# Performance work log

Hardware: AMD Instinct MI355X
Metric: run time of the kernel (lower is better)

Reference implementation:

```python
import jax, jax.numpy as jnp
import numpy as np

B, S, D = 2, 2048, 1024
H = 16
HD = D // H  # 64


def setup_inputs() -> dict:
    key = jax.random.key(0)
    ks = jax.random.split(key, 6)
    x = jax.random.normal(ks[0], (B, S, D), dtype=jnp.float32)
    sc = 1.0 / np.sqrt(D)
    Wq = jax.random.normal(ks[1], (D, D), dtype=jnp.float32) * sc
    Wk = jax.random.normal(ks[2], (D, D), dtype=jnp.float32) * sc
    Wv = jax.random.normal(ks[3], (D, D), dtype=jnp.float32) * sc
    Wo = jax.random.normal(ks[4], (D, D), dtype=jnp.float32) * sc
    bo = jax.random.normal(ks[5], (D,), dtype=jnp.float32) * 0.01
    return {"x": x, "Wq": Wq, "Wk": Wk, "Wv": Wv, "Wo": Wo, "bo": bo}


def reference(x, Wq, Wk, Wv, Wo, bo):
    b, s, d = x.shape
    # projections (torch Linear: y = x @ W.T; weights here stored as [d_in, d_out])
    Q = (x @ Wq).reshape(b, s, H, HD).transpose(0, 2, 1, 3)  # [b,h,s,hd]
    K = (x @ Wk).reshape(b, s, H, HD).transpose(0, 2, 1, 3)
    V = (x @ Wv).reshape(b, s, H, HD).transpose(0, 2, 1, 3)
    scores = jnp.einsum("bhqd,bhkd->bhqk", Q, K) / np.sqrt(HD)
    causal = jnp.triu(jnp.ones((s, s), dtype=bool), k=1)  # True above diagonal
    scores = jnp.where(causal[None, None], -jnp.inf, scores)
    attn = jax.nn.softmax(scores, axis=-1)
    # dropout_rate = 0.0 -> identity (eval-mode reference)
    ctx = jnp.einsum("bhqk,bhkd->bhqd", attn, V)
    ctx = ctx.transpose(0, 2, 1, 3).reshape(b, s, d)
    return ctx @ Wo + bo
```

## Files before the change

### kernel.cpp

```cpp
#include <hip/hip_runtime.h>
#include <hip/hip_bf16.h>

#define B_  2
#define S_  2048
#define D_  1024
#define H_  16
#define HD_ 64
#define M_  (B_*S_)

typedef __attribute__((ext_vector_type(8))) short short8;
typedef __attribute__((ext_vector_type(4))) float f32x4;

#define MFMA16(a, b, c) __builtin_amdgcn_mfma_f32_16x16x32_bf16((a), (b), (c), 0, 0, 0)

static __device__ inline short f2bf(float f) {
    union { float f; unsigned u; } v; v.f = f;
    unsigned r = v.u + 0x7FFFu + ((v.u >> 16) & 1u);
    return (short)(r >> 16);
}

static __device__ __forceinline__ float fexp2(float x) {
    float r;
    asm volatile("v_exp_f32 %0, %1\n\ts_nop 1" : "=v"(r) : "v"(x));
    return r;
}

static __device__ __forceinline__ unsigned cvt_pk_bf16(float lo, float hi) {
    unsigned r;
    asm volatile("v_cvt_pk_bf16_f32 %0, %1, %2" : "=v"(r) : "v"(lo), "v"(hi));
    return r;
}

static __device__ __forceinline__ void gl_lds16(const short* g, short* l) {
    __builtin_amdgcn_global_load_lds(
        (const __attribute__((address_space(1))) void*)g,
        (__attribute__((address_space(3))) void*)l, 16, 0, 0);
}

__global__ void cvt_x_kernel(const float* __restrict__ x, short* __restrict__ xb, int n4) {
    int i = blockIdx.x * blockDim.x + threadIdx.x;
    int stride = gridDim.x * blockDim.x;
    for (; i < n4; i += stride) {
        float4 v = ((const float4*)x)[i];
        short4 o;
        o.x = f2bf(v.x); o.y = f2bf(v.y); o.z = f2bf(v.z); o.w = f2bf(v.w);
        ((short4*)xb)[i] = o;
    }
}

__global__ void transpose_w4_kernel(const float* __restrict__ Wq, const float* __restrict__ Wk,
                                    const float* __restrict__ Wv, const float* __restrict__ Wo,
                                    short* __restrict__ Wqkvt, short* __restrict__ Wot) {
    __shared__ float tile[32][33];
    int z = blockIdx.z;
    const float* W = (z == 0) ? Wq : (z == 1) ? Wk : (z == 2) ? Wv : Wo;
    short* Wt = (z == 3) ? Wot : (Wqkvt + ((size_t)z << 20));
    int tx = threadIdx.x & 31, ty = threadIdx.x >> 5;
    int n0 = blockIdx.x * 32, k0 = blockIdx.y * 32;
#pragma unroll
    for (int i = 0; i < 4; ++i)
        tile[ty + 8 * i][tx] = W[(size_t)(k0 + ty + 8 * i) * D_ + n0 + tx];
    __syncthreads();
#pragma unroll
    for (int i = 0; i < 4; ++i)
        Wt[(size_t)(n0 + ty + 8 * i) * D_ + k0 + tx] = f2bf(tile[tx][ty + 8 * i]);
}

template <int MODE>
__global__ __launch_bounds__(256, 6) void gemm64(const short* __restrict__ A,
                                                 const short* __restrict__ Bt,
                                                 const float* __restrict__ bias,
                                                 void* __restrict__ out) {
    __shared__ __align__(16) short Asm[2][64 * 32];
    __shared__ __align__(16) short Bsm[2][128 * 32];
    int x = blockIdx.x & 7, wgl = blockIdx.x >> 3;
    int bm, bn;
    if (MODE == 0) { bn = x * 3 + (wgl >> 6); bm = wgl & 63; }
    else           { bn = x;                  bm = wgl;      }
    int tid = threadIdx.x, l = tid & 63, w = tid >> 6;
    int lhi = l >> 4, llo = l & 15;

    f32x4 acc[4][2];
#pragma unroll
    for (int m = 0; m < 4; ++m)
#pragma unroll
        for (int n = 0; n < 2; ++n) acc[m][n] = (f32x4){0.f, 0.f, 0.f, 0.f};

    const short* Ag = A + (size_t)(bm * 64) * 1024;
    const short* Bg = Bt + (size_t)(bn * 128) * 1024;
    int ca = tid;
    int ra = ((ca >> 5) << 3) | (ca & 7), sa = ((ca >> 3) & 3) ^ (ra & 3);
    int cb0 = tid, cb1 = tid + 256;
    int rb0 = ((cb0 >> 5) << 3) | (cb0 & 7), sb0 = ((cb0 >> 3) & 3) ^ (rb0 & 3);
    int rb1 = ((cb1 >> 5) << 3) | (cb1 & 7), sb1 = ((cb1 >> 3) & 3) ^ (rb1 & 3);

    auto stage = [&](int buf, int k0) {
        gl_lds16(Ag + (size_t)ra * 1024 + k0 + sa * 8, &Asm[buf][ca * 8]);
        gl_lds16(Bg + (size_t)rb0 * 1024 + k0 + sb0 * 8, &Bsm[buf][cb0 * 8]);
        gl_lds16(Bg + (size_t)rb1 * 1024 + k0 + sb1 * 8, &Bsm[buf][cb1 * 8]);
    };

    int cia[4], cib[2];
#pragma unroll
    for (int m = 0; m < 4; ++m) {
        int row = m * 16 + llo;
        cia[m] = ((row >> 3) << 5) | (((lhi ^ row) & 3) << 3) | (row & 7);
    }
#pragma unroll
    for (int n = 0; n < 2; ++n) {
        int row = w * 32 + n * 16 + llo;
        cib[n] = ((row >> 3) << 5) | (((lhi ^ row) & 3) << 3) | (row & 7);
    }

    stage(0, 0);
    for (int i = 0; i < 32; ++i) {
        asm volatile("s_waitcnt vmcnt(0)" ::: "memory");
        __builtin_amdgcn_s_barrier();
        asm volatile("" ::: "memory");
        if (i + 1 < 32) stage((i + 1) & 1, (i + 1) * 32);
        int cur = i & 1;
        short8 af[4], bf[2];
#pragma unroll
        for (int m = 0; m < 4; ++m) af[m] = *(const short8*)&Asm[cur][cia[m] * 8];
#pragma unroll
        for (int n = 0; n < 2; ++n) bf[n] = *(const short8*)&Bsm[cur][cib[n] * 8];
#pragma unroll
        for (int m = 0; m < 4; ++m)
#pragma unroll
            for (int n = 0; n < 2; ++n)
                acc[m][n] = MFMA16(af[m], bf[n], acc[m][n]);
    }

    int rowb = bm * 64, colb = bn * 128 + w * 32;
#pragma unroll
    for (int m = 0; m < 4; ++m) {
#pragma unroll
        for (int n = 0; n < 2; ++n) {
            int col = colb + n * 16 + llo;
#pragma unroll
            for (int j = 0; j < 4; ++j) {
                int row = rowb + m * 16 + lhi * 4 + j;
                float v = acc[m][n][j];
                if (MODE == 2) {
                    ((float*)out)[(size_t)row * 1024 + col] = v + bias[col];
                } else {
                    int proj = col >> 10, n1 = col & 1023;
                    int h = n1 >> 6, hd = n1 & 63;
                    int b = row >> 11, s = row & 2047;
                    short* o = (short*)out;
                    size_t off;
                    if (proj == 0)
                        off = ((size_t)(b * 16 + h) * 2048 + s) * 64 + hd;
                    else if (proj == 1)
                        off = (size_t)M_ * D_ + ((size_t)(b * 16 + h) * 2048 + s) * 64 + hd;
                    else
                        off = (size_t)2 * M_ * D_ + ((size_t)(b * 16 + h) * 64 + hd) * 2048 + s;
                    o[off] = f2bf(v);
                }
            }
        }
    }
}

__global__ __launch_bounds__(512) void attn_kernel(const short* __restrict__ Q,
                                                   const short* __restrict__ Kg,
                                                   const short* __restrict__ Vt,
                                                   short* __restrict__ ctx) {
    __shared__ __align__(16) char kvbuf[2][16384];
    __shared__ __align__(16) char plds[8][2048];
    int tid = threadIdx.x, w = tid >> 6, l = tid & 63;
    int lhi = l >> 4, llo = l & 15;
    int bh = blockIdx.x & 31, qp = blockIdx.x >> 5;
    int b = bh >> 4, h = bh & 15;
    char* pb = plds[w];

    const short* Qh = Q + (size_t)bh * S_ * HD_;
    const short* Kh = Kg + (size_t)bh * S_ * HD_;
    const short* Vh = Vt + (size_t)bh * HD_ * S_;

    int qbA = qp, qbB = 15 - qp;
    int NTA = 2 * qp + 2;
    const int NT = 34;

    int srow = tid >> 3;
    int ssrc = (16 * (tid & 7)) ^ ((srow & 7) << 4);
    auto stage = [&](char* buf, int c0) {
        gl_lds16(Kh + (size_t)(c0 + srow) * HD_ + (ssrc >> 1), (short*)(buf + tid * 16));
        gl_lds16(Vh + (size_t)srow * S_ + c0 + (ssrc >> 1), (short*)(buf + 8192 + tid * 16));
    };

    f32x4 O[4];
#pragma unroll
    for (int n = 0; n < 4; ++n) O[n] = (f32x4){0.f, 0.f, 0.f, 0.f};
    float lpart[4] = {0.f, 0.f, 0.f, 0.f};

    auto writeOut = [&](int qb) {
        int qbs = qb * 128 + w * 16;
#pragma unroll
        for (int j = 0; j < 4; ++j) {
            float ls = lpart[j];
            ls += __shfl_xor(ls, 1);
            ls += __shfl_xor(ls, 2);
            ls += __shfl_xor(ls, 4);
            ls += __shfl_xor(ls, 8);
            float inv = 1.0f / ls;
            int row = qbs + lhi * 4 + j;
            size_t base = ((size_t)(b * S_ + row)) * D_ + h * HD_;
#pragma unroll
            for (int n = 0; n < 4; ++n)
                ctx[base + n * 16 + llo] = f2bf(O[n][j] * inv);
        }
    };

    const float SC = 0.18033688f;
    const float M2 = 17.312340f;

    int qbase = qbA * 128 + w * 16;
    short8 aq0 = *(const short8*)(Qh + (size_t)(qbase + llo) * HD_ + 8 * lhi);
    short8 aq1 = *(const short8*)(Qh + (size_t)(qbase + llo) * HD_ + 32 + 8 * lhi);

    stage(kvbuf[0], 0);

    for (int i = 0; i < NT; ++i) {
        asm volatile("s_waitcnt vmcnt(0)" ::: "memory");
        __builtin_amdgcn_s_barrier();
        asm volatile("" ::: "memory");
        int kt = (i < NTA) ? i : i - NTA;
        int c0 = kt * 64;
        if (i + 1 < NT) {
            int ni = i + 1;
            int nkt = (ni < NTA) ? ni : ni - NTA;
            stage(kvbuf[ni & 1], nkt * 64);
        }
        const char* kb = kvbuf[i & 1];
        const char* vb = kb + 8192;

        if (c0 <= qbase + 15) {
            f32x4 sc4[4];
#pragma unroll
            for (int cb = 0; cb < 4; ++cb) {
                int row = cb * 16 + llo;
                int sw = (row & 7) << 4;
                short8 kf0 = *(const short8*)(kb + row * 128 + ((16 * lhi) ^ sw));
                short8 kf1 = *(const short8*)(kb + row * 128 + ((64 + 16 * lhi) ^ sw));
                f32x4 z = (f32x4){0.f, 0.f, 0.f, 0.f};
                z = MFMA16(aq0, kf0, z);
                z = MFMA16(aq1, kf1, z);
                sc4[cb] = z;
            }
            bool diag = (c0 + 63 > qbase);
#pragma unroll
            for (int j = 0; j < 4; ++j) {
                int qr = qbase + lhi * 4 + j;
                float v0 = fmaf(sc4[0][j], SC, -M2);
                float v1 = fmaf(sc4[1][j], SC, -M2);
                float v2 = fmaf(sc4[2][j], SC, -M2);
                float v3 = fmaf(sc4[3][j], SC, -M2);
                if (diag) {
                    if (c0 + llo > qr)      v0 = -1e30f;
                    if (c0 + 16 + llo > qr) v1 = -1e30f;
                    if (c0 + 32 + llo > qr) v2 = -1e30f;
                    if (c0 + 48 + llo > qr) v3 = -1e30f;
                }
                float p0 = fexp2(v0), p1 = fexp2(v1);
                float p2 = fexp2(v2), p3 = fexp2(v3);
                lpart[j] += (p0 + p1) + (p2 + p3);
                unsigned pk01 = cvt_pk_bf16(p0, p1);
                unsigned pk23 = cvt_pk_bf16(p2, p3);
                int r = lhi * 4 + j;
                char* rb = pb + r * 128;
                int sw = (r & 7) << 4;
                *(short*)(rb + ((2 * llo) ^ sw))      = (short)(pk01);
                *(short*)(rb + ((2 * llo + 32) ^ sw)) = (short)(pk01 >> 16);
                *(short*)(rb + ((2 * llo + 64) ^ sw)) = (short)(pk23);
                *(short*)(rb + ((2 * llo + 96) ^ sw)) = (short)(pk23 >> 16);
            }
            int swr = (llo & 7) << 4;
            short8 pa0 = *(const short8*)(pb + llo * 128 + ((16 * lhi) ^ swr));
            short8 pa1 = *(const short8*)(pb + llo * 128 + ((64 + 16 * lhi) ^ swr));
#pragma unroll
            for (int n = 0; n < 4; ++n) {
                int row = n * 16 + llo;
                int sw = (row & 7) << 4;
                short8 vf0 = *(const short8*)(vb + row * 128 + ((16 * lhi) ^ sw));
                short8 vf1 = *(const short8*)(vb + row * 128 + ((64 + 16 * lhi) ^ sw));
                O[n] = MFMA16(pa0, vf0, O[n]);
                O[n] = MFMA16(pa1, vf1, O[n]);
            }
        }

        if (i == NTA - 1) {
            writeOut(qbA);
#pragma unroll
            for (int n = 0; n < 4; ++n) O[n] = (f32x4){0.f, 0.f, 0.f, 0.f};
            lpart[0] = lpart[1] = lpart[2] = lpart[3] = 0.f;
            qbase = qbB * 128 + w * 16;
            aq0 = *(const short8*)(Qh + (size_t)(qbase + llo) * HD_ + 8 * lhi);
            aq1 = *(const short8*)(Qh + (size_t)(qbase + llo) * HD_ + 32 + 8 * lhi);
        }
    }
    writeOut(qbB);
}

extern "C" void kernel_launch(void* const* d_in, const int* in_sizes, int n_in,
                              void* d_out, int out_size, void* d_ws, size_t ws_size,
                              hipStream_t stream) {
    const float* x  = (const float*)d_in[0];
    const float* Wq = (const float*)d_in[1];
    const float* Wk = (const float*)d_in[2];
    const float* Wv = (const float*)d_in[3];
    const float* Wo = (const float*)d_in[4];
    const float* bo = (const float*)d_in[5];
    float* out = (float*)d_out;

    char* ws = (char*)d_ws;
    short* xb    = (short*)(ws);
    short* Wqkvt = (short*)(ws + (size_t)(8 << 20));
    short* Wot   = (short*)(ws + (size_t)(14 << 20));
    short* Qb    = (short*)(ws + (size_t)(16 << 20));
    short* Kb    = Qb + (size_t)M_ * D_;
    short* Vtb   = Qb + (size_t)2 * M_ * D_;
    short* ctx   = xb;

    cvt_x_kernel<<<2048, 256, 0, stream>>>(x, xb, M_ * D_ / 4);
    transpose_w4_kernel<<<dim3(32, 32, 4), 256, 0, stream>>>(Wq, Wk, Wv, Wo, Wqkvt, Wot);

    gemm64<0><<<1536, 256, 0, stream>>>(xb, Wqkvt, nullptr, Qb);
    attn_kernel<<<256, 512, 0, stream>>>(Qb, Kb, Vtb, ctx);
    gemm64<2><<<512, 256, 0, stream>>>(ctx, Wot, bo, out);
}
```

Before: 140.2 us.

## Replace QKV projection GEMM with 256x256-tile, 8-wave kernel using K=64 stages

The fused QKV projection moves from a 64x128 tile GEMM with 1536 small blocks to a dedicated kernel with 256x256 output tiles, 512 threads (8 waves in a 2x4 grid) and K-step 64, using direct global-to-LDS loads with an XOR swizzle. Larger tiles raise arithmetic intensity and cut redundant global/L2 traffic for A and B. In exchange, only 192 blocks run (fewer than the CU count, so some CUs idle), each block needs 128KB of LDS, and register pressure is high from the 128 accumulator floats per lane. The output projection keeps the old kernel under a new non-templated name.

```diff
diff --git a/kernel.cpp b/kernel.cpp
--- a/kernel.cpp
+++ b/kernel.cpp
@@ -66,17 +66,114 @@
         Wt[(size_t)(n0 + ty + 8 * i) * D_ + k0 + tx] = f2bf(tile[tx][ty + 8 * i]);
 }
 
-template <int MODE>
-__global__ __launch_bounds__(256, 6) void gemm64(const short* __restrict__ A,
-                                                 const short* __restrict__ Bt,
-                                                 const float* __restrict__ bias,
-                                                 void* __restrict__ out) {
+__global__ __launch_bounds__(512, 2) void gemm_qkv8(const short* __restrict__ A,
+                                                    const short* __restrict__ Bt,
+                                                    short* __restrict__ out) {
+    __shared__ __align__(16) short Als[2][256 * 64];
+    __shared__ __align__(16) short Bls[2][256 * 64];
+    int x = blockIdx.x & 7, wgl = blockIdx.x >> 3;
+    int wg = x * 24 + wgl;
+    int bn = wg / 16, bm = wg % 16;
+    int tid = threadIdx.x, l = tid & 63, w = tid >> 6;
+    int lhi = l >> 4, llo = l & 15;
+    int wm = w >> 2, wn = w & 3;
+
+    f32x4 acc[8][4];
+#pragma unroll
+    for (int m = 0; m < 8; ++m)
+#pragma unroll
+        for (int n = 0; n < 4; ++n) acc[m][n] = (f32x4){0.f, 0.f, 0.f, 0.f};
+
+    const short* Ag = A + (size_t)(bm * 256) * 1024;
+    const short* Bg = Bt + (size_t)(bn * 256) * 1024;
+
+    int rowp[4], sp[4];
+#pragma unroll
+    for (int p = 0; p < 4; ++p) {
+        int c = p * 512 + tid;
+        rowp[p] = ((c >> 6) << 3) | (c & 7);
+        sp[p] = ((c >> 3) & 7) ^ (rowp[p] & 7);
+    }
+    auto cidx = [](int row, int s) {
+        return ((row >> 3) << 6) | (((s ^ row) & 7) << 3) | (row & 7);
+    };
+
+#pragma unroll
+    for (int p = 0; p < 4; ++p) {
+        gl_lds16(Ag + (size_t)rowp[p] * 1024 + sp[p] * 8, &Als[0][(p * 512 + tid) * 8]);
+        gl_lds16(Bg + (size_t)rowp[p] * 1024 + sp[p] * 8, &Bls[0][(p * 512 + tid) * 8]);
+    }
+
+    for (int t = 0; t < 16; ++t) {
+        asm volatile("s_waitcnt vmcnt(0)" ::: "memory");
+        __builtin_amdgcn_s_barrier();
+        asm volatile("" ::: "memory");
+        int cur = t & 1, nxt = cur ^ 1;
+        short8 bf[4];
+#pragma unroll
+        for (int p = 0; p < 4; ++p) {
+            if (t + 1 < 16) {
+                gl_lds16(Ag + (size_t)rowp[p] * 1024 + (t + 1) * 64 + sp[p] * 8,
+                         &Als[nxt][(p * 512 + tid) * 8]);
+                gl_lds16(Bg + (size_t)rowp[p] * 1024 + (t + 1) * 64 + sp[p] * 8,
+                         &Bls[nxt][(p * 512 + tid) * 8]);
+            }
+            int kk = p >> 1, mh = p & 1;
+            if (mh == 0) {
+#pragma unroll
+                for (int nf = 0; nf < 4; ++nf) {
+                    int row = wn * 64 + nf * 16 + llo, s = kk * 4 + lhi;
+                    bf[nf] = *(const short8*)&Bls[cur][cidx(row, s) * 8];
+                }
+            }
+            short8 af[4];
+#pragma unroll
+            for (int mf = 0; mf < 4; ++mf) {
+                int row = wm * 128 + (mh * 4 + mf) * 16 + llo, s = kk * 4 + lhi;
+                af[mf] = *(const short8*)&Als[cur][cidx(row, s) * 8];
+            }
+#pragma unroll
+            for (int mf = 0; mf < 4; ++mf)
+#pragma unroll
+                for (int nf = 0; nf < 4; ++nf)
+                    acc[mh * 4 + mf][nf] = MFMA16(af[mf], bf[nf], acc[mh * 4 + mf][nf]);
+        }
+    }
+
+    int rowb = bm * 256 + wm * 128, colb = bn * 256 + wn * 64;
+#pragma unroll
+    for (int f = 0; f < 8; ++f) {
+#pragma unroll
+        for (int nf = 0; nf < 4; ++nf) {
+            int col = colb + nf * 16 + llo;
+#pragma unroll
+            for (int j = 0; j < 4; ++j) {
+                int row = rowb + f * 16 + lhi * 4 + j;
+                float v = acc[f][nf][j];
+                int proj = col >> 10, n1 = col & 1023;
+                int h = n1 >> 6, hd = n1 & 63;
+                int b = row >> 11, s = row & 2047;
+                size_t off;
+                if (proj == 0)
+                    off = ((size_t)(b * 16 + h) * 2048 + s) * 64 + hd;
+                else if (proj == 1)
+                    off = (size_t)M_ * D_ + ((size_t)(b * 16 + h) * 2048 + s) * 64 + hd;
+                else
+                    off = (size_t)2 * M_ * D_ + ((size_t)(b * 16 + h) * 64 + hd) * 2048 + s;
+                out[off] = f2bf(v);
+            }
+        }
+    }
+}
+
+__global__ __launch_bounds__(256, 6) void gemm_out(const short* __restrict__ A,
+                                                   const short* __restrict__ Bt,
+                                                   const float* __restrict__ bias,
+                                                   float* __restrict__ out) {
     __shared__ __align__(16) short Asm[2][64 * 32];
     __shared__ __align__(16) short Bsm[2][128 * 32];
     int x = blockIdx.x & 7, wgl = blockIdx.x >> 3;
-    int bm, bn;
-    if (MODE == 0) { bn = x * 3 + (wgl >> 6); bm = wgl & 63; }
-    else           { bn = x;                  bm = wgl;      }
+    int bn = x, bm = wgl;
     int tid = threadIdx.x, l = tid & 63, w = tid >> 6;
     int lhi = l >> 4, llo = l & 15;
 
@@ -133,33 +230,16 @@
 
     int rowb = bm * 64, colb = bn * 128 + w * 32;
 #pragma unroll
-    for (int m = 0; m < 4; ++m) {
+    for (int m = 0; m < 4; ++m)
 #pragma unroll
         for (int n = 0; n < 2; ++n) {
             int col = colb + n * 16 + llo;
 #pragma unroll
             for (int j = 0; j < 4; ++j) {
                 int row = rowb + m * 16 + lhi * 4 + j;
-                float v = acc[m][n][j];
-                if (MODE == 2) {
-                    ((float*)out)[(size_t)row * 1024 + col] = v + bias[col];
-                } else {
-                    int proj = col >> 10, n1 = col & 1023;
-                    int h = n1 >> 6, hd = n1 & 63;
-                    int b = row >> 11, s = row & 2047;
-                    short* o = (short*)out;
-                    size_t off;
-                    if (proj == 0)
-                        off = ((size_t)(b * 16 + h) * 2048 + s) * 64 + hd;
-                    else if (proj == 1)
-                        off = (size_t)M_ * D_ + ((size_t)(b * 16 + h) * 2048 + s) * 64 + hd;
-                    else
-                        off = (size_t)2 * M_ * D_ + ((size_t)(b * 16 + h) * 64 + hd) * 2048 + s;
-                    o[off] = f2bf(v);
-                }
-            }
-        }
-    }
+                out[(size_t)row * 1024 + col] = acc[m][n][j] + bias[col];
+            }
+        }
 }
 
 __global__ __launch_bounds__(512) void attn_kernel(const short* __restrict__ Q,
@@ -325,7 +405,7 @@
     cvt_x_kernel<<<2048, 256, 0, stream>>>(x, xb, M_ * D_ / 4);
     transpose_w4_kernel<<<dim3(32, 32, 4), 256, 0, stream>>>(Wq, Wk, Wv, Wo, Wqkvt, Wot);
 
-    gemm64<0><<<1536, 256, 0, stream>>>(xb, Wqkvt, nullptr, Qb);
+    gemm_qkv8<<<192, 512, 0, stream>>>(xb, Wqkvt, Qb);
     attn_kernel<<<256, 512, 0, stream>>>(Qb, Kb, Vtb, ctx);
-    gemm64<2><<<512, 256, 0, stream>>>(ctx, Wot, bo, out);
-}
+    gemm_out<<<512, 256, 0, stream>>>(ctx, Wot, bo, out);
+}
```

Measured after the change: 153.6 us. 9.6% more time.
